# Kernel tuning notes

Measured on AMD Instinct MI355X. Metric: run time of the kernel, lower is better.

The kernel has to match this reference:

```python
import jax, jax.numpy as jnp
import numpy as np

TAU = 1.0  # current_temp buffer (temperature=1.0)

def setup_inputs() -> dict:
    key = jax.random.key(0)
    ks = jax.random.split(key, 6)
    B, T, d, L, H = 4, 64, 128, 32, 32  # H = hidden_dim // 2
    z_signal = jax.random.normal(ks[0], (B, T, d, L), dtype=jnp.float32)
    W_mag = jax.random.normal(ks[1], (d, d), dtype=jnp.float32) * 0.01  # init_scale
    W1 = jax.random.normal(ks[2], (H, 2 * L), dtype=jnp.float32) * (1.0 / np.sqrt(2 * L))
    b1 = jax.random.normal(ks[3], (H,), dtype=jnp.float32) * 0.01
    W2 = jax.random.normal(ks[4], (1, H), dtype=jnp.float32) * (1.0 / np.sqrt(H))
    b2 = jax.random.normal(ks[5], (1,), dtype=jnp.float32) * 0.01
    return {"z_signal": z_signal, "W_mag": W_mag, "W1": W1, "b1": b1, "W2": W2, "b2": b2}

def reference(z_signal, W_mag, W1, b1, W2, b2):
    B, T, d, L = z_signal.shape
    h = z_signal.reshape(B * T, d, L)  # [N, d, L]
    # Linear(2L,H) on cat(h_i, h_j) == h_i @ W1a.T + h_j @ W1b.T (decomposed, same math)
    W1a, W1b = W1[:, :L], W1[:, L:]
    pa = jnp.einsum('ndl,hl->ndh', h, W1a)  # contribution of h_i
    pb = jnp.einsum('ndl,hl->ndh', h, W1b)  # contribution of h_j
    hidden = jax.nn.relu(pa[:, :, None, :] + pb[:, None, :, :] + b1)  # [N, d, d, H]
    scores = jnp.einsum('nijh,h->nij', hidden, W2[0]) + b2[0]          # [N, d, d]
    antisym = scores - jnp.swapaxes(scores, -1, -2)
    antisym_logits = antisym.mean(axis=0)                              # [d, d]
    eye = jnp.eye(d, dtype=z_signal.dtype)
    dir_probs = jax.nn.sigmoid(antisym_logits / TAU) * (1.0 - eye)
    # symmetric magnitude with zero diagonal
    Wm = 0.5 * (W_mag + W_mag.T) * (1.0 - eye)
    A = jax.nn.sigmoid(Wm) * dir_probs * (1.0 - eye)
    return (A, Wm)
```

## Files before the change

### kernel.cpp

```cpp
#include <hip/hip_runtime.h>
#include <hip/hip_bf16.h>
#include <math.h>

#define D     128
#define NT    256
#define HD    32
#define LD    32
#define PADW  132
#define STW   136
#define TILES 136
#define NSLAB (TILES * 64)

static __device__ inline unsigned short f2bf(float f) {
    __hip_bfloat16 b = __float2bfloat16(f);
    return *reinterpret_cast<unsigned short*>(&b);
}
static __device__ inline float bf2f(unsigned int u16v) {
    union { unsigned int i; float f; } v;
    v.i = u16v << 16;
    return v.f;
}

union SmemA {
    float zt[LD][PADW];
    float lin[2][D];
};
union SmemB {
    struct { float spa[HD][PADW]; float spb[HD][PADW]; } p;
    unsigned short st[D][STW];
};

__global__ __launch_bounds__(512) void fused_pab_scores(
    const float* __restrict__ z, const float* __restrict__ W1,
    const float* __restrict__ b1, const float* __restrict__ W2,
    unsigned short* __restrict__ Dp)
{
    __shared__ SmemA sa;
    __shared__ SmemB sb;

    const int t = threadIdx.x;
    const int n = blockIdx.x;

    {
        const float4* zsrc = (const float4*)(z + (size_t)n * (D * LD));
        #pragma unroll
        for (int q = 0; q < 2; ++q) {
            int f = t + q * 512;
            float4 v = zsrc[f];
            int i = f >> 3;
            int l = (f & 7) * 4;
            sa.zt[l + 0][i] = v.x; sa.zt[l + 1][i] = v.y;
            sa.zt[l + 2][i] = v.z; sa.zt[l + 3][i] = v.w;
        }
    }

    const int h  = t & 31;
    const int iq = t >> 5;
    float wa[LD], wb[LD];
    #pragma unroll
    for (int k = 0; k < 8; ++k) {
        *(float4*)&wa[k*4] = *(const float4*)&W1[h * 64 + k*4];
        *(float4*)&wb[k*4] = *(const float4*)&W1[h * 64 + 32 + k*4];
    }
    const float bias = b1[h];
    __syncthreads();

    {
        float a[8], c[8];
        #pragma unroll
        for (int r = 0; r < 8; ++r) { a[r] = bias; c[r] = 0.f; }
        #pragma unroll
        for (int l = 0; l < LD; ++l) {
            float4 z0 = *(const float4*)&sa.zt[l][iq * 8];
            float4 z1 = *(const float4*)&sa.zt[l][iq * 8 + 4];
            float zr[8] = {z0.x, z0.y, z0.z, z0.w, z1.x, z1.y, z1.z, z1.w};
            #pragma unroll
            for (int r = 0; r < 8; ++r) {
                a[r] = fmaf(zr[r], wa[l], a[r]);
                c[r] = fmaf(zr[r], wb[l], c[r]);
            }
        }
        *(float4*)&sb.p.spa[h][iq * 8]     = make_float4(a[0], a[1], a[2], a[3]);
        *(float4*)&sb.p.spa[h][iq * 8 + 4] = make_float4(a[4], a[5], a[6], a[7]);
        *(float4*)&sb.p.spb[h][iq * 8]     = make_float4(c[0], c[1], c[2], c[3]);
        *(float4*)&sb.p.spb[h][iq * 8 + 4] = make_float4(c[4], c[5], c[6], c[7]);
    }

    float w2r[HD];
    #pragma unroll
    for (int q = 0; q < HD; ++q) w2r[q] = 0.5f * W2[q];
    __syncthreads();

    if (t < 256) {
        const int kind = t >> 7, i2 = t & 127;
        float s = 0.f;
        #pragma unroll
        for (int hq = 0; hq < HD; ++hq) {
            float v = kind ? sb.p.spb[hq][i2] : sb.p.spa[hq][i2];
            s = fmaf(w2r[hq], v, s);
        }
        sa.lin[kind][i2] = s;
    }

    const int tx = t & 31;
    const int ty = t >> 5;
    float acc[8][4];
    #pragma unroll
    for (int r = 0; r < 8; ++r)
        #pragma unroll
        for (int c = 0; c < 4; ++c) acc[r][c] = 0.f;

    #pragma unroll 4
    for (int hh = 0; hh < HD; ++hh) {
        float4 a0 = *(const float4*)&sb.p.spa[hh][ty * 8];
        float4 a1 = *(const float4*)&sb.p.spa[hh][ty * 8 + 4];
        float4 bv = *(const float4*)&sb.p.spb[hh][tx * 4];
        const float w = w2r[hh];
        float ar[8] = {a0.x, a0.y, a0.z, a0.w, a1.x, a1.y, a1.z, a1.w};
        float br[4] = {bv.x, bv.y, bv.z, bv.w};
        #pragma unroll
        for (int r = 0; r < 8; ++r)
            #pragma unroll
            for (int c = 0; c < 4; ++c)
                acc[r][c] = fmaf(w, fabsf(ar[r] + br[c]), acc[r][c]);
    }
    __syncthreads();

    {
        float cai[8], cbj[4];
        #pragma unroll
        for (int r = 0; r < 8; ++r) cai[r] = sa.lin[0][ty * 8 + r];
        #pragma unroll
        for (int c = 0; c < 4; ++c) cbj[c] = sa.lin[1][tx * 4 + c];
        #pragma unroll
        for (int r = 0; r < 8; ++r)
            #pragma unroll
            for (int c = 0; c < 4; ++c)
                acc[r][c] += cai[r] + cbj[c];
    }

    const int jo = tx >> 1;
    const int jh = tx & 1;
    {
        const int physW = ((jo ^ (ty & 7)) * 8) + jh * 4;
        #pragma unroll
        for (int r = 0; r < 8; ++r) {
            unsigned int p0 = ((unsigned int)f2bf(acc[r][1]) << 16) | f2bf(acc[r][0]);
            unsigned int p1 = ((unsigned int)f2bf(acc[r][3]) << 16) | f2bf(acc[r][2]);
            *(uint2*)&sb.st[ty * 8 + r][physW] = make_uint2(p0, p1);
        }
    }
    __syncthreads();

    if (jo >= ty) {
        float sji[4][8];
        const int physR = (ty ^ (jo & 7)) * 8;
        #pragma unroll
        for (int c = 0; c < 4; ++c) {
            const int j = jo * 8 + jh * 4 + c;
            uint4 u = *(const uint4*)&sb.st[j][physR];
            unsigned int xs[4] = {u.x, u.y, u.z, u.w};
            #pragma unroll
            for (int k = 0; k < 4; ++k) {
                sji[c][2*k]   = bf2f(xs[k] & 0xffff);
                sji[c][2*k+1] = bf2f(xs[k] >> 16);
            }
        }
        const int tidx = ty * 16 - (ty * (ty - 1)) / 2 + (jo - ty);
        unsigned short* Dn = Dp + (size_t)n * NSLAB + tidx * 64;
        #pragma unroll
        for (int r = 0; r < 8; ++r) {
            unsigned short l0 = f2bf(acc[r][0] - sji[0][r]);
            unsigned short l1 = f2bf(acc[r][1] - sji[1][r]);
            unsigned short l2 = f2bf(acc[r][2] - sji[2][r]);
            unsigned short l3 = f2bf(acc[r][3] - sji[3][r]);
            unsigned int p0 = ((unsigned int)l1 << 16) | l0;
            unsigned int p1 = ((unsigned int)l3 << 16) | l2;
            *(uint2*)&Dn[r * 8 + jh * 4] = make_uint2(p0, p1);
        }
    }
}

__global__ __launch_bounds__(256) void finalize_tiles(
    const unsigned short* __restrict__ Dp, const float* __restrict__ Wmag,
    float* __restrict__ out)
{
    __shared__ float red[32][72];

    const int b = blockIdx.x;
    int tq = 0, base = 0;
    while (b >= base + (16 - tq)) { base += 16 - tq; ++tq; }
    const int tp = tq + (b - base);

    const int t = threadIdx.x;
    const int g = t >> 3;
    const int s = t & 7;

    float a8[8] = {0.f, 0.f, 0.f, 0.f, 0.f, 0.f, 0.f, 0.f};
    #pragma unroll 2
    for (int q = 0; q < 8; ++q) {
        const int nn = g * 8 + q;
        uint4 u = *(const uint4*)&Dp[(size_t)nn * NSLAB + b * 64 + s * 8];
        unsigned int xs[4] = {u.x, u.y, u.z, u.w};
        #pragma unroll
        for (int k = 0; k < 4; ++k) {
            a8[2*k]   += bf2f(xs[k] & 0xffff);
            a8[2*k+1] += bf2f(xs[k] >> 16);
        }
    }
    *(float4*)&red[g][s * 8]     = make_float4(a8[0], a8[1], a8[2], a8[3]);
    *(float4*)&red[g][s * 8 + 4] = make_float4(a8[4], a8[5], a8[6], a8[7]);
    __syncthreads();

    if (t < 64) {
        const int r = t >> 3, c = t & 7;
        float sum = 0.f;
        #pragma unroll 8
        for (int gg = 0; gg < 32; ++gg) sum += red[gg][t];

        const int i = 8 * tq + r;
        const int j = 8 * tp + c;
        if (i == j) {
            out[i * D + i]         = 0.f;
            out[D * D + i * D + i] = 0.f;
        } else if (j > i) {
            float av  = sum * (1.0f / 256.0f);
            float dir = 1.0f / (1.0f + __expf(-av));
            float wmm = 0.5f * (Wmag[i * D + j] + Wmag[j * D + i]);
            float sw  = 1.0f / (1.0f + __expf(-wmm));
            out[i * D + j]         = dir * sw;
            out[j * D + i]         = (1.0f - dir) * sw;
            out[D * D + i * D + j] = wmm;
            out[D * D + j * D + i] = wmm;
        }
    }
}

extern "C" void kernel_launch(void* const* d_in, const int* in_sizes, int n_in,
                              void* d_out, int out_size, void* d_ws, size_t ws_size,
                              hipStream_t stream)
{
    const float* z    = (const float*)d_in[0];
    const float* Wmag = (const float*)d_in[1];
    const float* W1   = (const float*)d_in[2];
    const float* b1   = (const float*)d_in[3];
    const float* W2   = (const float*)d_in[4];

    unsigned short* Dp = (unsigned short*)d_ws;
    float* out = (float*)d_out;

    fused_pab_scores<<<NT, 512, 0, stream>>>(z, W1, b1, W2, Dp);
    finalize_tiles<<<TILES, 256, 0, stream>>>(Dp, Wmag, out);
}
```

Measured before the change: 29.26 us.

## Switch projection and pairwise score math to packed fp16 with fdot2

Stores z, the projected hidden activations and W1/W2 as packed half2 values. The projection, linear term and pairwise |a+b| accumulation then use packed fp16 adds, a sign mask and v_dot2 fp32-accumulate instructions, which halves both the LDS footprint and the ALU op count of the dominant inner loop. The cost is reduced precision: the hidden pre-activations are rounded to fp16 before the abs-sum, which may perturb the antisymmetric logits.

Result: faster. 28.19 us (-3.7%).

```diff
diff --git a/kernel.cpp b/kernel.cpp
--- a/kernel.cpp
+++ b/kernel.cpp
@@ -6,10 +6,12 @@
 #define NT    256
 #define HD    32
 #define LD    32
-#define PADW  132
+#define P32   132
 #define STW   136
 #define TILES 136
 #define NSLAB (TILES * 64)
+
+typedef _Float16 h2v __attribute__((ext_vector_type(2)));
 
 static __device__ inline unsigned short f2bf(float f) {
     __hip_bfloat16 b = __float2bfloat16(f);
@@ -20,13 +22,28 @@
     v.i = u16v << 16;
     return v.f;
 }
+static __device__ inline unsigned int pkh2(float a, float b) {
+    union { h2v h; unsigned int u; } cv;
+    cv.h = (h2v){(_Float16)a, (_Float16)b};
+    return cv.u;
+}
+static __device__ inline h2v u2h(unsigned int u) {
+    union { unsigned int u; h2v h; } cv; cv.u = u; return cv.h;
+}
+static __device__ inline float fdot2f(h2v a, h2v b, float c) {
+#if __has_builtin(__builtin_amdgcn_fdot2)
+    return __builtin_amdgcn_fdot2(a, b, c, false);
+#else
+    return c + (float)a[0] * (float)b[0] + (float)a[1] * (float)b[1];
+#endif
+}
 
 union SmemA {
-    float zt[LD][PADW];
+    unsigned int zt[16][P32];
     float lin[2][D];
 };
 union SmemB {
-    struct { float spa[HD][PADW]; float spb[HD][PADW]; } p;
+    struct { unsigned int a[16][P32]; unsigned int b[16][P32]; } p;
     unsigned short st[D][STW];
 };
 
@@ -47,57 +64,71 @@
         for (int q = 0; q < 2; ++q) {
             int f = t + q * 512;
             float4 v = zsrc[f];
-            int i = f >> 3;
-            int l = (f & 7) * 4;
-            sa.zt[l + 0][i] = v.x; sa.zt[l + 1][i] = v.y;
-            sa.zt[l + 2][i] = v.z; sa.zt[l + 3][i] = v.w;
-        }
-    }
-
-    const int h  = t & 31;
-    const int iq = t >> 5;
-    float wa[LD], wb[LD];
+            int i  = f >> 3;
+            int l2 = (f & 7) * 2;
+            sa.zt[l2][i]     = pkh2(v.x, v.y);
+            sa.zt[l2 + 1][i] = pkh2(v.z, v.w);
+        }
+    }
+
+    const int h2i = t & 15;
+    const int iq  = t >> 4;
+    const int h0 = 2 * h2i, h1 = h0 + 1;
+    unsigned int wpkA0[16], wpkA1[16], wpkB0[16], wpkB1[16];
+    {
+        const float* w1r0 = &W1[h0 * 64];
+        const float* w1r1 = &W1[h1 * 64];
+        #pragma unroll
+        for (int l2 = 0; l2 < 16; ++l2) {
+            wpkA0[l2] = pkh2(w1r0[2*l2],      w1r0[2*l2 + 1]);
+            wpkB0[l2] = pkh2(w1r0[32 + 2*l2], w1r0[32 + 2*l2 + 1]);
+            wpkA1[l2] = pkh2(w1r1[2*l2],      w1r1[2*l2 + 1]);
+            wpkB1[l2] = pkh2(w1r1[32 + 2*l2], w1r1[32 + 2*l2 + 1]);
+        }
+    }
+    const float bias0 = b1[h0], bias1 = b1[h1];
+
+    unsigned int w2pk[16];
     #pragma unroll
-    for (int k = 0; k < 8; ++k) {
-        *(float4*)&wa[k*4] = *(const float4*)&W1[h * 64 + k*4];
-        *(float4*)&wb[k*4] = *(const float4*)&W1[h * 64 + 32 + k*4];
-    }
-    const float bias = b1[h];
-    __syncthreads();
-
-    {
-        float a[8], c[8];
-        #pragma unroll
-        for (int r = 0; r < 8; ++r) { a[r] = bias; c[r] = 0.f; }
-        #pragma unroll
-        for (int l = 0; l < LD; ++l) {
-            float4 z0 = *(const float4*)&sa.zt[l][iq * 8];
-            float4 z1 = *(const float4*)&sa.zt[l][iq * 8 + 4];
-            float zr[8] = {z0.x, z0.y, z0.z, z0.w, z1.x, z1.y, z1.z, z1.w};
-            #pragma unroll
-            for (int r = 0; r < 8; ++r) {
-                a[r] = fmaf(zr[r], wa[l], a[r]);
-                c[r] = fmaf(zr[r], wb[l], c[r]);
+    for (int q = 0; q < 16; ++q)
+        w2pk[q] = pkh2(0.5f * W2[2*q], 0.5f * W2[2*q + 1]);
+    __syncthreads();
+
+    {
+        float A0[4], A1[4], B0[4], B1[4];
+        #pragma unroll
+        for (int r = 0; r < 4; ++r) { A0[r] = bias0; A1[r] = bias1; B0[r] = 0.f; B1[r] = 0.f; }
+        #pragma unroll
+        for (int l2 = 0; l2 < 16; ++l2) {
+            unsigned int zq[4];
+            *(uint4*)zq = *(const uint4*)&sa.zt[l2][iq * 4];
+            #pragma unroll
+            for (int r = 0; r < 4; ++r) {
+                h2v zv = u2h(zq[r]);
+                A0[r] = fdot2f(zv, u2h(wpkA0[l2]), A0[r]);
+                A1[r] = fdot2f(zv, u2h(wpkA1[l2]), A1[r]);
+                B0[r] = fdot2f(zv, u2h(wpkB0[l2]), B0[r]);
+                B1[r] = fdot2f(zv, u2h(wpkB1[l2]), B1[r]);
             }
         }
-        *(float4*)&sb.p.spa[h][iq * 8]     = make_float4(a[0], a[1], a[2], a[3]);
-        *(float4*)&sb.p.spa[h][iq * 8 + 4] = make_float4(a[4], a[5], a[6], a[7]);
-        *(float4*)&sb.p.spb[h][iq * 8]     = make_float4(c[0], c[1], c[2], c[3]);
-        *(float4*)&sb.p.spb[h][iq * 8 + 4] = make_float4(c[4], c[5], c[6], c[7]);
-    }
-
-    float w2r[HD];
-    #pragma unroll
-    for (int q = 0; q < HD; ++q) w2r[q] = 0.5f * W2[q];
+        unsigned int pa4[4], pb4[4];
+        #pragma unroll
+        for (int r = 0; r < 4; ++r) {
+            pa4[r] = pkh2(A0[r], A1[r]);
+            pb4[r] = pkh2(B0[r], B1[r]);
+        }
+        *(uint4*)&sb.p.a[h2i][iq * 4] = *(uint4*)pa4;
+        *(uint4*)&sb.p.b[h2i][iq * 4] = *(uint4*)pb4;
+    }
     __syncthreads();
 
     if (t < 256) {
         const int kind = t >> 7, i2 = t & 127;
         float s = 0.f;
         #pragma unroll
-        for (int hq = 0; hq < HD; ++hq) {
-            float v = kind ? sb.p.spb[hq][i2] : sb.p.spa[hq][i2];
-            s = fmaf(w2r[hq], v, s);
+        for (int q = 0; q < 16; ++q) {
+            unsigned int v = kind ? sb.p.b[q][i2] : sb.p.a[q][i2];
+            s = fdot2f(u2h(v), u2h(w2pk[q]), s);
         }
         sa.lin[kind][i2] = s;
     }
@@ -111,18 +142,23 @@
         for (int c = 0; c < 4; ++c) acc[r][c] = 0.f;
 
     #pragma unroll 4
-    for (int hh = 0; hh < HD; ++hh) {
-        float4 a0 = *(const float4*)&sb.p.spa[hh][ty * 8];
-        float4 a1 = *(const float4*)&sb.p.spa[hh][ty * 8 + 4];
-        float4 bv = *(const float4*)&sb.p.spb[hh][tx * 4];
-        const float w = w2r[hh];
-        float ar[8] = {a0.x, a0.y, a0.z, a0.w, a1.x, a1.y, a1.z, a1.w};
-        float br[4] = {bv.x, bv.y, bv.z, bv.w};
-        #pragma unroll
-        for (int r = 0; r < 8; ++r)
-            #pragma unroll
-            for (int c = 0; c < 4; ++c)
-                acc[r][c] = fmaf(w, fabsf(ar[r] + br[c]), acc[r][c]);
+    for (int q = 0; q < 16; ++q) {
+        unsigned int a8[8], b4[4];
+        *(uint4*)&a8[0] = *(const uint4*)&sb.p.a[q][ty * 8];
+        *(uint4*)&a8[4] = *(const uint4*)&sb.p.a[q][ty * 8 + 4];
+        *(uint4*)&b4[0] = *(const uint4*)&sb.p.b[q][tx * 4];
+        const h2v w = u2h(w2pk[q]);
+        #pragma unroll
+        for (int r = 0; r < 8; ++r) {
+            const h2v ha = u2h(a8[r]);
+            #pragma unroll
+            for (int c = 0; c < 4; ++c) {
+                union { h2v h; unsigned int u; } cv;
+                cv.h = ha + u2h(b4[c]);
+                cv.u &= 0x7fff7fffu;
+                acc[r][c] = fdot2f(cv.h, w, acc[r][c]);
+            }
+        }
     }
     __syncthreads();
 
```
